# Kernel optimization log

Hardware: AMD Instinct MI355X
Metric: run time of the kernel (lower is better)

## Reference

```python
import jax, jax.numpy as jnp
import numpy as np

B, C, D, H, W = 4, 1, 128, 192, 192


def setup_inputs() -> dict:
    key = jax.random.key(0)
    ks = jax.random.split(key, 8)
    x = jax.random.normal(ks[0], (B, C, D, H, W), jnp.float32)
    y = jax.random.normal(ks[1], (B, C, H, W), jnp.float32)
    rot_0 = jax.random.normal(ks[2], (B, 1), jnp.float32) * 0.1
    rot_1 = jax.random.normal(ks[3], (B, 1), jnp.float32) * 0.1
    rot_2 = jax.random.normal(ks[4], (B, 1), jnp.float32) * 0.1
    trans_1 = jax.random.normal(ks[5], (B, 1), jnp.float32) * 0.05
    trans_2 = jax.random.normal(ks[6], (B, 1), jnp.float32) * 0.05
    center_point = (jnp.tile(jnp.array([[D / 2., H / 2., W / 2.]], jnp.float32), (B, 1))
                    + jax.random.normal(ks[7], (B, 3), jnp.float32))
    return {"x": x, "y": y, "rot_0": rot_0, "rot_1": rot_1, "rot_2": rot_2,
            "trans_1": trans_1, "trans_2": trans_2, "center_point": center_point}


def _euler2mat(a):
    # a: [B,3] angles (z, y, x), ZYX intrinsic composition as in source
    z, y, x = a[:, 0], a[:, 1], a[:, 2]
    cz, sz = jnp.cos(z), jnp.sin(z)
    cy, sy = jnp.cos(y), jnp.sin(y)
    cx, sx = jnp.cos(x), jnp.sin(x)
    o = jnp.ones_like(z)
    zr = jnp.zeros_like(z)
    zmat = jnp.stack([cz, -sz, zr, sz, cz, zr, zr, zr, o], 1).reshape(-1, 3, 3)
    ymat = jnp.stack([cy, zr, sy, zr, o, zr, -sy, zr, cy], 1).reshape(-1, 3, 3)
    xmat = jnp.stack([o, zr, zr, zr, cx, -sx, zr, sx, cx], 1).reshape(-1, 3, 3)
    return zmat @ ymat @ xmat


def _rigid4x4(rot3, t):
    # rot3: [B,3,3], t: [B,3] -> [B,4,4]
    bn = rot3.shape[0]
    top = jnp.concatenate([rot3, t[:, :, None]], axis=-1)          # [B,3,4]
    bot = jnp.broadcast_to(jnp.array([[[0., 0., 0., 1.]]], jnp.float32), (bn, 1, 4))
    return jnp.concatenate([top, bot], axis=1)


def _trans_mat(t):
    bn = t.shape[0]
    eye = jnp.broadcast_to(jnp.eye(3, dtype=jnp.float32), (bn, 3, 3))
    return _rigid4x4(eye, t)


def _affine_grid(mat, shape):
    # mat: [B,4,4]; voxel-coordinate grid (nitorch convention): g = R @ c + t
    d, h, w = shape
    zz, yy, xx = jnp.meshgrid(jnp.arange(d, dtype=jnp.float32),
                              jnp.arange(h, dtype=jnp.float32),
                              jnp.arange(w, dtype=jnp.float32), indexing='ij')
    coords = jnp.stack([zz, yy, xx], axis=-1)                      # [D,H,W,3]
    return (jnp.einsum('dhwj,bij->bdhwi', coords, mat[:, :3, :3])
            + mat[:, None, None, None, :3, 3])                    # [B,D,H,W,3]


def _grid_pull_one(vol, g):
    # vol: [C,D,H,W]; g: [D,H,W,3] voxel coords; trilinear, zero boundary
    d, h, w = vol.shape[1], vol.shape[2], vol.shape[3]
    g0f = jnp.floor(g)
    frac = g - g0f
    g0 = g0f.astype(jnp.int32)
    out = jnp.zeros((vol.shape[0],) + g.shape[:-1], vol.dtype)
    for dz in (0, 1):
        wz = frac[..., 0] if dz else 1. - frac[..., 0]
        iz = g0[..., 0] + dz
        for dy in (0, 1):
            wy = frac[..., 1] if dy else 1. - frac[..., 1]
            iy = g0[..., 1] + dy
            for dx in (0, 1):
                wx = frac[..., 2] if dx else 1. - frac[..., 2]
                ix = g0[..., 2] + dx
                valid = ((iz >= 0) & (iz < d) & (iy >= 0) & (iy < h)
                         & (ix >= 0) & (ix < w)).astype(vol.dtype)
                v = vol[:, jnp.clip(iz, 0, d - 1), jnp.clip(iy, 0, h - 1),
                        jnp.clip(ix, 0, w - 1)]                   # [C,D,H,W]
                out = out + v * (wz * wy * wx * valid)[None]
    return out


def reference(x, y, rot_0, rot_1, rot_2, trans_1, trans_2, center_point):
    d, h, w = x.shape[2], x.shape[3], x.shape[4]
    t1 = _trans_mat(-center_point)
    t2 = _trans_mat(center_point)
    # first translation component is detached*0 -> exact zeros
    trans = jnp.concatenate([jnp.zeros_like(trans_1), trans_1 * h, trans_2 * w], axis=1)
    angles = jnp.concatenate([rot_0, rot_1, rot_2], axis=1)
    rot = _euler2mat(angles)
    rigid = _rigid4x4(rot, trans)
    mat = t2 @ (rigid @ t1)                                        # center-about-point rigid
    grid = _affine_grid(mat, (d, h, w))                            # [B,D,H,W,3]
    x_warp = jax.vmap(_grid_pull_one)(x, grid)                     # [B,C,D,H,W]
    x_2d = jnp.mean(x_warp, axis=2)                                # [B,C,H,W]
    return (x_2d, x_warp, y)
```

## Files before the change

### kernel.cpp

```cpp
#include <hip/hip_runtime.h>

#define Bn 4
#define Dd 128
#define Hh 192
#define Ww 192

#define PLANE (Hh * Ww)
#define VOL   (Dd * PLANE)
#define N2D   (Bn * PLANE)
#define WARP_OFF ((size_t)N2D)
#define Y_OFF (WARP_OFF + (size_t)Bn * VOL)

#define DT 16
#define HT 8
#define WT 32
#define NDB (Dd / DT)
#define NHB (Hh / HT)
#define NWB (Ww / WT)
#define NBLK (Bn * NDB * NHB * NWB)
#define NCH (NDB * 2)

#define SZ 25
#define SY 16
#define SXP 48
#define ZSTRIDE (SY * SXP)
#define LDSF (SZ * ZSTRIDE)

typedef float f2 __attribute__((ext_vector_type(2)));
typedef f2 __attribute__((aligned(4))) f2u;
__device__ __forceinline__ f2 load2(const float* p) { return *(const f2u*)p; }

__device__ __forceinline__ void gload_lds16(const float* g, float* l) {
    __builtin_amdgcn_global_load_lds(
        (const __attribute__((address_space(1))) void*)g,
        (__attribute__((address_space(3))) void*)l,
        16, 0, 0);
}

__global__ __launch_bounds__(256) void tbl_kernel(const float* __restrict__ rot0,
                                                  const float* __restrict__ rot1,
                                                  const float* __restrict__ rot2,
                                                  const float* __restrict__ tr1,
                                                  const float* __restrict__ tr2,
                                                  const float* __restrict__ cp,
                                                  float* __restrict__ tbl) {
    const int id = blockIdx.x * 256 + threadIdx.x;
    if (id >= NBLK) return;
    const int wblk = id % NWB;
    const int t1   = id / NWB;
    const int hblk = t1 % NHB;
    const int t2   = t1 / NHB;
    const int dblk = t2 & (NDB - 1);
    const int b    = t2 >> 3;

    const float z = rot0[b], y = rot1[b], x = rot2[b];
    const float cz = cosf(z), sz = sinf(z);
    const float cy = cosf(y), sy = sinf(y);
    const float cx = cosf(x), sx = sinf(x);
    const float A0 = cz * cy;
    const float B0 = -sz * cx + cz * sy * sx;
    const float C0 = sz * sx + cz * sy * cx;
    const float A1 = sz * cy;
    const float B1 = cz * cx + sz * sy * sx;
    const float C1 = -cz * sx + sz * sy * cx;
    const float A2 = -sy;
    const float B2 = cy * sx;
    const float C2 = cy * cx;
    const float c0 = cp[b * 3 + 0], c1 = cp[b * 3 + 1], c2 = cp[b * 3 + 2];
    const float E0 = -(A0 * c0 + B0 * c1 + C0 * c2) + c0;
    const float E1 = -(A1 * c0 + B1 * c1 + C1 * c2) + tr1[b] * (float)Hh + c1;
    const float E2 = -(A2 * c0 + B2 * c1 + C2 * c2) + tr2[b] * (float)Ww + c2;

    const int d0 = dblk * DT, h0 = hblk * HT, w0 = wblk * WT;
    const float dlo = (float)d0, dhi = (float)(d0 + DT - 1);
    const float hlo = (float)h0, hhi = (float)(h0 + HT - 1);
    const float wlo = (float)w0, whi = (float)(w0 + WT - 1);

    const float loZ = E0 + fminf(A0 * dlo, A0 * dhi) + fminf(B0 * hlo, B0 * hhi) + fminf(C0 * wlo, C0 * whi);
    const float hiZ = E0 + fmaxf(A0 * dlo, A0 * dhi) + fmaxf(B0 * hlo, B0 * hhi) + fmaxf(C0 * wlo, C0 * whi);
    const float loY = E1 + fminf(A1 * dlo, A1 * dhi) + fminf(B1 * hlo, B1 * hhi) + fminf(C1 * wlo, C1 * whi);
    const float hiY = E1 + fmaxf(A1 * dlo, A1 * dhi) + fmaxf(B1 * hlo, B1 * hhi) + fmaxf(C1 * wlo, C1 * whi);
    const float loX = E2 + fminf(A2 * dlo, A2 * dhi) + fminf(B2 * hlo, B2 * hhi) + fminf(C2 * wlo, C2 * whi);
    const float hiX = E2 + fmaxf(A2 * dlo, A2 * dhi) + fmaxf(B2 * hlo, B2 * hhi) + fmaxf(C2 * wlo, C2 * whi);

    const int lz = (int)floorf(loZ) - 1;
    const int hz = (int)floorf(hiZ) + 2;
    const int ly = (int)floorf(loY) - 1;
    const int hy = (int)floorf(hiY) + 2;
    const int lx4 = ((int)floorf(loX) - 1) & ~3;
    const int hx = (int)floorf(hiX) + 2;

    const int hzrel = hz - lz;
    const bool fits = (hzrel <= SZ - 1) && (hy - ly <= SY - 1) && (hx - lx4 <= SXP - 2);
    const bool interior = (loZ >= 0.01f) && (hiZ < (float)(Dd - 1) - 0.01f) &&
                          (loY >= 0.01f) && (hiY < (float)(Hh - 1) - 0.01f) &&
                          (loX >= 0.01f) && (hiX < (float)(Ww - 1) - 0.01f);

    const float bz = E0 + A0 * dlo + B0 * hlo + C0 * wlo - (float)lz;
    const float by = E1 + A1 * dlo + B1 * hlo + C1 * wlo - (float)ly;
    const float bx = E2 + A2 * dlo + B2 * hlo + C2 * wlo - (float)lx4;

    float* T = tbl + (size_t)id * 16;
    T[0] = A0; T[1] = B0; T[2]  = C0; T[3]  = bz;
    T[4] = A1; T[5] = B1; T[6]  = C1; T[7]  = by;
    T[8] = A2; T[9] = B2; T[10] = C2; T[11] = bx;
    int* TI = (int*)T;
    TI[12] = lz; TI[13] = ly; TI[14] = lx4;
    TI[15] = (fits ? 1 : 0) | (interior ? 2 : 0) |
             (b << 2) | (dblk << 4) | (hblk << 7) | (wblk << 12) | (min(hzrel, 127) << 15);
}

template <bool WP>
__global__ __launch_bounds__(512) void warp_tiled(const float* __restrict__ x,
                                                  const float* __restrict__ tbl,
                                                  float* __restrict__ out,
                                                  float* __restrict__ partial) {
    __shared__ __align__(16) float box[LDSF];

    const int g  = blockIdx.x;
    const int wl = (g & 7) * (NBLK / 8) + (g >> 3);

    const float4* T4 = (const float4*)(tbl + (size_t)wl * 16);
    const float4 r0 = T4[0], r1 = T4[1], r2 = T4[2];
    const int4   r3 = ((const int4*)T4)[3];
    const int lz = r3.x, ly = r3.y, lx4 = r3.z, fl = r3.w;
    const bool fits = fl & 1, interior = fl & 2;
    const int b     = (fl >> 2) & 3;
    const int dblk  = (fl >> 4) & 7;
    const int hblk  = (fl >> 7) & 31;
    const int wblk  = (fl >> 12) & 7;
    const int hzrel = (fl >> 15) & 127;
    const int d0 = dblk * DT, h0 = hblk * HT, w0 = wblk * WT;

    const float A0 = r0.x, B0 = r0.y, C0 = r0.z, bz = r0.w;
    const float A1 = r1.x, B1 = r1.y, C1 = r1.z, by = r1.w;
    const float A2 = r2.x, B2 = r2.y, C2 = r2.z, bx = r2.w;

    const int t = threadIdx.x;
    const int w_in = t & 31;
    const int h_in = (t >> 5) & 7;
    const int dq   = t >> 8;
    const int lane = t & 63;
    const int wid  = t >> 6;

    const float fh = (float)h_in, fw = (float)w_in, fdq = (float)(dq * 8);
    const float fz0 = bz + B0 * fh + C0 * fw + A0 * fdq;
    const float fy0 = by + B1 * fh + C1 * fw + A1 * fdq;
    const float fx0 = bx + B2 * fh + C2 * fw + A2 * fdq;

    const float* __restrict__ V = x + (size_t)b * VOL;
    float* __restrict__ obase = out + WARP_OFF + (size_t)b * VOL +
                                (size_t)(d0 + dq * 8) * PLANE +
                                (size_t)(h0 + h_in) * Ww + (w0 + w_in);

    float sum = 0.0f;

    if (fits) {
        const int r0i = lane / 12,             c0i = (lane - r0i * 12) * 4;
        const int i1  = 64 + lane;  const int r1i = i1 / 12, c1i = (i1 - r1i * 12) * 4;
        const int i2  = 128 + lane; const int r2i = i2 / 12, c2i = (i2 - r2i * 12) * 4;
        const int yy0 = ly + r0i, xx0 = lx4 + c0i;
        const int yy1 = ly + r1i, xx1 = lx4 + c1i;
        const int yy2 = ly + r2i, xx2 = lx4 + c2i;
        const bool ok0 = ((unsigned)yy0 < (unsigned)Hh) && ((unsigned)xx0 <= (unsigned)(Ww - 4));
        const bool ok1 = ((unsigned)yy1 < (unsigned)Hh) && ((unsigned)xx1 <= (unsigned)(Ww - 4));
        const bool ok2 = ((unsigned)yy2 < (unsigned)Hh) && ((unsigned)xx2 <= (unsigned)(Ww - 4));
        const int off0 = yy0 * Ww + xx0;
        const int off1 = yy1 * Ww + xx1;
        const int off2 = yy2 * Ww + xx2;

        if (!interior) {
            const float4 z4 = {0.0f, 0.0f, 0.0f, 0.0f};
            for (int i = 4 * t; i < LDSF; i += 4 * 512) *(float4*)&box[i] = z4;
            __syncthreads();
        }

        for (int zrel = wid; zrel <= hzrel; zrel += 8) {
            const int zz = lz + zrel;
            if ((unsigned)zz < (unsigned)Dd) {
                const float* Vz = V + (size_t)zz * PLANE;
                float* Lz = box + zrel * ZSTRIDE;
                if (ok0) gload_lds16(Vz + off0, Lz);
                if (ok1) gload_lds16(Vz + off1, Lz + 256);
                if (ok2) gload_lds16(Vz + off2, Lz + 512);
            }
        }

        int   basev[8];
        float txv[8], tyv[8], tzv[8];
        #pragma unroll
        for (int j = 0; j < 8; ++j) {
            const float fd = (float)j;
            const float gz = fmaf(A0, fd, fz0);
            const float gy = fmaf(A1, fd, fy0);
            const float gx = fmaf(A2, fd, fx0);
            const float fz = floorf(gz), fy = floorf(gy), fx = floorf(gx);
            tzv[j] = gz - fz; tyv[j] = gy - fy; txv[j] = gx - fx;
            basev[j] = (int)fz * ZSTRIDE + (int)fy * SXP + (int)fx;
        }
        __syncthreads();

        #pragma unroll
        for (int j = 0; j < 8; ++j) {
            const int base = basev[j];
            const f2 qa = load2(&box[base]);
            const f2 qb = load2(&box[base + SXP]);
            const f2 qc = load2(&box[base + ZSTRIDE]);
            const f2 qd = load2(&box[base + ZSTRIDE + SXP]);

            const float tx = txv[j], ty = tyv[j], tz = tzv[j];
            const float wx0 = 1.0f - tx, wy0 = 1.0f - ty, wz0 = 1.0f - tz;
            const float v00 = fmaf(wx0, qa.x, tx * qa.y);
            const float v01 = fmaf(wx0, qb.x, tx * qb.y);
            const float v10 = fmaf(wx0, qc.x, tx * qc.y);
            const float v11 = fmaf(wx0, qd.x, tx * qd.y);
            const float vz0 = fmaf(wy0, v00, ty * v01);
            const float vz1 = fmaf(wy0, v10, ty * v11);
            const float val = fmaf(wz0, vz0, tz * vz1);

            __builtin_nontemporal_store(val, obase + (size_t)j * PLANE);
            sum += val;
        }
    } else {
        const float fz0a = fz0 + (float)lz;
        const float fy0a = fy0 + (float)ly;
        const float fx0a = fx0 + (float)lx4;
        #pragma unroll 4
        for (int j = 0; j < 8; ++j) {
            const float fd = (float)j;
            const float gz = fmaf(A0, fd, fz0a);
            const float gy = fmaf(A1, fd, fy0a);
            const float gx = fmaf(A2, fd, fx0a);

            const float fz = floorf(gz), fy = floorf(gy), fx = floorf(gx);
            const float tz = gz - fz, ty = gy - fy, tx = gx - fx;
            const int iz = (int)fz, iy = (int)fy, ix = (int)fx;

            const float wz0 = ((unsigned)iz       < (unsigned)Dd) ? (1.0f - tz) : 0.0f;
            const float wz1 = ((unsigned)(iz + 1) < (unsigned)Dd) ? tz : 0.0f;
            const float wy0 = ((unsigned)iy       < (unsigned)Hh) ? (1.0f - ty) : 0.0f;
            const float wy1 = ((unsigned)(iy + 1) < (unsigned)Hh) ? ty : 0.0f;
            const float wx0 = ((unsigned)ix       < (unsigned)Ww) ? (1.0f - tx) : 0.0f;
            const float wx1 = ((unsigned)(ix + 1) < (unsigned)Ww) ? tx : 0.0f;

            const bool right  = (ix >= Ww - 1);
            const bool leftok = (ix >= 0);
            const float WL = (right ? 0.0f : wx0) + (leftok ? 0.0f : wx1);
            const float WH = (right ? wx0 : 0.0f) + (leftok ? wx1 : 0.0f);

            const int iz0c = min(max(iz, 0), Dd - 1);
            const int iz1c = min(max(iz + 1, 0), Dd - 1);
            const int iy0c = min(max(iy, 0), Hh - 1);
            const int iy1c = min(max(iy + 1, 0), Hh - 1);
            const int ixl  = min(max(ix, 0), Ww - 2);

            const f2 q00 = load2(V + (size_t)iz0c * PLANE + iy0c * Ww + ixl);
            const f2 q01 = load2(V + (size_t)iz0c * PLANE + iy1c * Ww + ixl);
            const f2 q10 = load2(V + (size_t)iz1c * PLANE + iy0c * Ww + ixl);
            const f2 q11 = load2(V + (size_t)iz1c * PLANE + iy1c * Ww + ixl);

            const float v00 = fmaf(WL, q00.x, WH * q00.y);
            const float v01 = fmaf(WL, q01.x, WH * q01.y);
            const float v10 = fmaf(WL, q10.x, WH * q10.y);
            const float v11 = fmaf(WL, q11.x, WH * q11.y);

            const float vz0 = fmaf(wy0, v00, wy1 * v01);
            const float vz1 = fmaf(wy0, v10, wy1 * v11);
            const float val = fmaf(wz0, vz0, wz1 * vz1);

            __builtin_nontemporal_store(val, obase + (size_t)j * PLANE);
            sum += val;
        }
    }

    if (WP) {
        const int ch = dblk * 2 + dq;
        partial[((size_t)(b * NCH + ch) * Hh + (h0 + h_in)) * Ww + (w0 + w_in)] = sum;
    }
}

__global__ __launch_bounds__(256) void reduce_kernel(const float* __restrict__ partial,
                                                     const float* __restrict__ yin,
                                                     float* __restrict__ out) {
    const int idx = blockIdx.x * 256 + threadIdx.x;
    if (idx >= N2D) return;
    const int b = idx / PLANE;
    const int rem = idx - b * PLANE;
    const float* p = partial + (size_t)b * NCH * PLANE + rem;
    float s = 0.0f;
    #pragma unroll
    for (int c = 0; c < NCH; ++c) s += p[(size_t)c * PLANE];
    out[idx] = s * (1.0f / (float)Dd);
    out[Y_OFF + idx] = yin[idx];
}

__global__ __launch_bounds__(256) void reduce_fallback_kernel(const float* __restrict__ yin,
                                                              float* __restrict__ out) {
    const int idx = blockIdx.x * 256 + threadIdx.x;
    if (idx >= N2D) return;
    const int b = idx / PLANE;
    const int rem = idx - b * PLANE;
    const float* p = out + WARP_OFF + (size_t)b * VOL + rem;
    float s = 0.0f;
    #pragma unroll 8
    for (int d = 0; d < Dd; ++d) s += p[(size_t)d * PLANE];
    out[idx] = s * (1.0f / (float)Dd);
    out[Y_OFF + idx] = yin[idx];
}

extern "C" void kernel_launch(void* const* d_in, const int* in_sizes, int n_in,
                              void* d_out, int out_size, void* d_ws, size_t ws_size,
                              hipStream_t stream) {
    const float* x    = (const float*)d_in[0];
    const float* yin  = (const float*)d_in[1];
    const float* rot0 = (const float*)d_in[2];
    const float* rot1 = (const float*)d_in[3];
    const float* rot2 = (const float*)d_in[4];
    const float* tr1  = (const float*)d_in[5];
    const float* tr2  = (const float*)d_in[6];
    const float* cp   = (const float*)d_in[7];

    float* tbl = (float*)d_ws;
    float* partial = tbl + (size_t)NBLK * 16;
    const size_t need = ((size_t)NBLK * 16 + (size_t)Bn * NCH * PLANE) * sizeof(float);

    tbl_kernel<<<(NBLK + 255) / 256, 256, 0, stream>>>(rot0, rot1, rot2, tr1, tr2, cp, tbl);

    if (ws_size >= need) {
        warp_tiled<true><<<NBLK, 512, 0, stream>>>(x, tbl, (float*)d_out, partial);
        reduce_kernel<<<(N2D + 255) / 256, 256, 0, stream>>>(partial, yin, (float*)d_out);
    } else {
        warp_tiled<false><<<NBLK, 512, 0, stream>>>(x, tbl, (float*)d_out, partial);
        reduce_fallback_kernel<<<(N2D + 255) / 256, 256, 0, stream>>>(yin, (float*)d_out);
    }
}
```

Measured before the change: 50.64 us.

## Split each warp tile into two depth phases with smaller LDS box

The per-block 16-deep tile is now processed in two sequential 8-deep phases, each with its own bounding-box table entry. This shrinks the LDS staging box from 25 to 17 z-slices, which raises how many blocks fit per CU and tightens the loaded halo per phase. The cost is an extra barrier between phases and serialized load/compute inside each block. The reduce kernel is also vectorized to float4 loads and stores.

```diff
diff --git a/kernel.cpp b/kernel.cpp
--- a/kernel.cpp
+++ b/kernel.cpp
@@ -18,9 +18,10 @@
 #define NHB (Hh / HT)
 #define NWB (Ww / WT)
 #define NBLK (Bn * NDB * NHB * NWB)
+#define NTBL (NBLK * 2)
 #define NCH (NDB * 2)
 
-#define SZ 25
+#define SZ 17
 #define SY 16
 #define SXP 48
 #define ZSTRIDE (SY * SXP)
@@ -45,9 +46,11 @@
                                                   const float* __restrict__ cp,
                                                   float* __restrict__ tbl) {
     const int id = blockIdx.x * 256 + threadIdx.x;
-    if (id >= NBLK) return;
-    const int wblk = id % NWB;
-    const int t1   = id / NWB;
+    if (id >= NTBL) return;
+    const int wl    = id >> 1;
+    const int phase = id & 1;
+    const int wblk = wl % NWB;
+    const int t1   = wl / NWB;
     const int hblk = t1 % NHB;
     const int t2   = t1 / NHB;
     const int dblk = t2 & (NDB - 1);
@@ -71,8 +74,9 @@
     const float E1 = -(A1 * c0 + B1 * c1 + C1 * c2) + tr1[b] * (float)Hh + c1;
     const float E2 = -(A2 * c0 + B2 * c1 + C2 * c2) + tr2[b] * (float)Ww + c2;
 
-    const int d0 = dblk * DT, h0 = hblk * HT, w0 = wblk * WT;
-    const float dlo = (float)d0, dhi = (float)(d0 + DT - 1);
+    const int d0 = dblk * DT + phase * 8;
+    const int h0 = hblk * HT, w0 = wblk * WT;
+    const float dlo = (float)d0, dhi = (float)(d0 + 7);
     const float hlo = (float)h0, hhi = (float)(h0 + HT - 1);
     const float wlo = (float)w0, whi = (float)(w0 + WT - 1);
 
@@ -120,22 +124,6 @@
     const int g  = blockIdx.x;
     const int wl = (g & 7) * (NBLK / 8) + (g >> 3);
 
-    const float4* T4 = (const float4*)(tbl + (size_t)wl * 16);
-    const float4 r0 = T4[0], r1 = T4[1], r2 = T4[2];
-    const int4   r3 = ((const int4*)T4)[3];
-    const int lz = r3.x, ly = r3.y, lx4 = r3.z, fl = r3.w;
-    const bool fits = fl & 1, interior = fl & 2;
-    const int b     = (fl >> 2) & 3;
-    const int dblk  = (fl >> 4) & 7;
-    const int hblk  = (fl >> 7) & 31;
-    const int wblk  = (fl >> 12) & 7;
-    const int hzrel = (fl >> 15) & 127;
-    const int d0 = dblk * DT, h0 = hblk * HT, w0 = wblk * WT;
-
-    const float A0 = r0.x, B0 = r0.y, C0 = r0.z, bz = r0.w;
-    const float A1 = r1.x, B1 = r1.y, C1 = r1.z, by = r1.w;
-    const float A2 = r2.x, B2 = r2.y, C2 = r2.z, bx = r2.w;
-
     const int t = threadIdx.x;
     const int w_in = t & 31;
     const int h_in = (t >> 5) & 7;
@@ -143,155 +131,186 @@
     const int lane = t & 63;
     const int wid  = t >> 6;
 
-    const float fh = (float)h_in, fw = (float)w_in, fdq = (float)(dq * 8);
-    const float fz0 = bz + B0 * fh + C0 * fw + A0 * fdq;
-    const float fy0 = by + B1 * fh + C1 * fw + A1 * fdq;
-    const float fx0 = bx + B2 * fh + C2 * fw + A2 * fdq;
-
-    const float* __restrict__ V = x + (size_t)b * VOL;
-    float* __restrict__ obase = out + WARP_OFF + (size_t)b * VOL +
-                                (size_t)(d0 + dq * 8) * PLANE +
-                                (size_t)(h0 + h_in) * Ww + (w0 + w_in);
+    const int r0i = lane / 12,             c0i = (lane - r0i * 12) * 4;
+    const int i1  = 64 + lane;  const int r1i = i1 / 12, c1i = (i1 - r1i * 12) * 4;
+    const int i2  = 128 + lane; const int r2i = i2 / 12, c2i = (i2 - r2i * 12) * 4;
 
     float sum = 0.0f;
-
-    if (fits) {
-        const int r0i = lane / 12,             c0i = (lane - r0i * 12) * 4;
-        const int i1  = 64 + lane;  const int r1i = i1 / 12, c1i = (i1 - r1i * 12) * 4;
-        const int i2  = 128 + lane; const int r2i = i2 / 12, c2i = (i2 - r2i * 12) * 4;
-        const int yy0 = ly + r0i, xx0 = lx4 + c0i;
-        const int yy1 = ly + r1i, xx1 = lx4 + c1i;
-        const int yy2 = ly + r2i, xx2 = lx4 + c2i;
-        const bool ok0 = ((unsigned)yy0 < (unsigned)Hh) && ((unsigned)xx0 <= (unsigned)(Ww - 4));
-        const bool ok1 = ((unsigned)yy1 < (unsigned)Hh) && ((unsigned)xx1 <= (unsigned)(Ww - 4));
-        const bool ok2 = ((unsigned)yy2 < (unsigned)Hh) && ((unsigned)xx2 <= (unsigned)(Ww - 4));
-        const int off0 = yy0 * Ww + xx0;
-        const int off1 = yy1 * Ww + xx1;
-        const int off2 = yy2 * Ww + xx2;
-
-        if (!interior) {
-            const float4 z4 = {0.0f, 0.0f, 0.0f, 0.0f};
-            for (int i = 4 * t; i < LDSF; i += 4 * 512) *(float4*)&box[i] = z4;
+    int bO = 0, dblkO = 0, h0O = 0, w0O = 0;
+
+    #pragma unroll 1
+    for (int ph = 0; ph < 2; ++ph) {
+        const float4* T4 = (const float4*)(tbl + ((size_t)wl * 2 + ph) * 16);
+        const float4 r0 = T4[0], r1 = T4[1], r2 = T4[2];
+        const int4   r3 = ((const int4*)T4)[3];
+        const int lz = r3.x, ly = r3.y, lx4 = r3.z, fl = r3.w;
+        const bool fits = fl & 1, interior = fl & 2;
+        const int b     = (fl >> 2) & 3;
+        const int dblk  = (fl >> 4) & 7;
+        const int hblk  = (fl >> 7) & 31;
+        const int wblk  = (fl >> 12) & 7;
+        const int hzrel = (fl >> 15) & 127;
+        const int h0 = hblk * HT, w0 = wblk * WT;
+        const int d0 = dblk * DT + ph * 8;
+        bO = b; dblkO = dblk; h0O = h0; w0O = w0;
+
+        const float A0 = r0.x, B0 = r0.y, C0 = r0.z, bz = r0.w;
+        const float A1 = r1.x, B1 = r1.y, C1 = r1.z, by = r1.w;
+        const float A2 = r2.x, B2 = r2.y, C2 = r2.z, bx = r2.w;
+
+        const float fh = (float)h_in, fw = (float)w_in, fdq = (float)(dq * 4);
+        const float fz0 = bz + B0 * fh + C0 * fw + A0 * fdq;
+        const float fy0 = by + B1 * fh + C1 * fw + A1 * fdq;
+        const float fx0 = bx + B2 * fh + C2 * fw + A2 * fdq;
+
+        const float* __restrict__ V = x + (size_t)b * VOL;
+        float* __restrict__ obase = out + WARP_OFF + (size_t)b * VOL +
+                                    (size_t)(d0 + dq * 4) * PLANE +
+                                    (size_t)(h0 + h_in) * Ww + (w0 + w_in);
+
+        if (fits) {
+            const int yy0 = ly + r0i, xx0 = lx4 + c0i;
+            const int yy1 = ly + r1i, xx1 = lx4 + c1i;
+            const int yy2 = ly + r2i, xx2 = lx4 + c2i;
+            const bool ok0 = ((unsigned)yy0 < (unsigned)Hh) && ((unsigned)xx0 <= (unsigned)(Ww - 4));
+            const bool ok1 = ((unsigned)yy1 < (unsigned)Hh) && ((unsigned)xx1 <= (unsigned)(Ww - 4));
+            const bool ok2 = ((unsigned)yy2 < (unsigned)Hh) && ((unsigned)xx2 <= (unsigned)(Ww - 4));
+            const int off0 = yy0 * Ww + xx0;
+            const int off1 = yy1 * Ww + xx1;
+            const int off2 = yy2 * Ww + xx2;
+
+            if (!interior) {
+                const float4 z4 = {0.0f, 0.0f, 0.0f, 0.0f};
+                for (int i = 4 * t; i < LDSF; i += 4 * 512) *(float4*)&box[i] = z4;
+                __syncthreads();
+            }
+
+            for (int zrel = wid; zrel <= hzrel; zrel += 8) {
+                const int zz = lz + zrel;
+                if ((unsigned)zz < (unsigned)Dd) {
+                    const float* Vz = V + (size_t)zz * PLANE;
+                    float* Lz = box + zrel * ZSTRIDE;
+                    if (ok0) gload_lds16(Vz + off0, Lz);
+                    if (ok1) gload_lds16(Vz + off1, Lz + 256);
+                    if (ok2) gload_lds16(Vz + off2, Lz + 512);
+                }
+            }
+
+            int   basev[4];
+            float txv[4], tyv[4], tzv[4];
+            #pragma unroll
+            for (int j = 0; j < 4; ++j) {
+                const float fd = (float)j;
+                const float gz = fmaf(A0, fd, fz0);
+                const float gy = fmaf(A1, fd, fy0);
+                const float gx = fmaf(A2, fd, fx0);
+                const float fz = floorf(gz), fy = floorf(gy), fx = floorf(gx);
+                tzv[j] = gz - fz; tyv[j] = gy - fy; txv[j] = gx - fx;
+                basev[j] = (int)fz * ZSTRIDE + (int)fy * SXP + (int)fx;
+            }
             __syncthreads();
+
+            #pragma unroll
+            for (int j = 0; j < 4; ++j) {
+                const int base = basev[j];
+                const f2 qa = load2(&box[base]);
+                const f2 qb = load2(&box[base + SXP]);
+                const f2 qc = load2(&box[base + ZSTRIDE]);
+                const f2 qd = load2(&box[base + ZSTRIDE + SXP]);
+
+                const float tx = txv[j], ty = tyv[j], tz = tzv[j];
+                const float wx0 = 1.0f - tx, wy0 = 1.0f - ty, wz0 = 1.0f - tz;
+                const float v00 = fmaf(wx0, qa.x, tx * qa.y);
+                const float v01 = fmaf(wx0, qb.x, tx * qb.y);
+                const float v10 = fmaf(wx0, qc.x, tx * qc.y);
+                const float v11 = fmaf(wx0, qd.x, tx * qd.y);
+                const float vz0 = fmaf(wy0, v00, ty * v01);
+                const float vz1 = fmaf(wy0, v10, ty * v11);
+                const float val = fmaf(wz0, vz0, tz * vz1);
+
+                __builtin_nontemporal_store(val, obase + (size_t)j * PLANE);
+                sum += val;
+            }
+        } else {
+            const float fz0a = fz0 + (float)lz;
+            const float fy0a = fy0 + (float)ly;
+            const float fx0a = fx0 + (float)lx4;
+            #pragma unroll
+            for (int j = 0; j < 4; ++j) {
+                const float fd = (float)j;
+                const float gz = fmaf(A0, fd, fz0a);
+                const float gy = fmaf(A1, fd, fy0a);
+                const float gx = fmaf(A2, fd, fx0a);
+
+                const float fz = floorf(gz), fy = floorf(gy), fx = floorf(gx);
+                const float tz = gz - fz, ty = gy - fy, tx = gx - fx;
+                const int iz = (int)fz, iy = (int)fy, ix = (int)fx;
+
+                const float wz0 = ((unsigned)iz       < (unsigned)Dd) ? (1.0f - tz) : 0.0f;
+                const float wz1 = ((unsigned)(iz + 1) < (unsigned)Dd) ? tz : 0.0f;
+                const float wy0 = ((unsigned)iy       < (unsigned)Hh) ? (1.0f - ty) : 0.0f;
+                const float wy1 = ((unsigned)(iy + 1) < (unsigned)Hh) ? ty : 0.0f;
+                const float wx0 = ((unsigned)ix       < (unsigned)Ww) ? (1.0f - tx) : 0.0f;
+                const float wx1 = ((unsigned)(ix + 1) < (unsigned)Ww) ? tx : 0.0f;
+
+                const bool right  = (ix >= Ww - 1);
+                const bool leftok = (ix >= 0);
+                const float WL = (right ? 0.0f : wx0) + (leftok ? 0.0f : wx1);
+                const float WH = (right ? wx0 : 0.0f) + (leftok ? wx1 : 0.0f);
+
+                const int iz0c = min(max(iz, 0), Dd - 1);
+                const int iz1c = min(max(iz + 1, 0), Dd - 1);
+                const int iy0c = min(max(iy, 0), Hh - 1);
+                const int iy1c = min(max(iy + 1, 0), Hh - 1);
+                const int ixl  = min(max(ix, 0), Ww - 2);
+
+                const f2 q00 = load2(V + (size_t)iz0c * PLANE + iy0c * Ww + ixl);
+                const f2 q01 = load2(V + (size_t)iz0c * PLANE + iy1c * Ww + ixl);
+                const f2 q10 = load2(V + (size_t)iz1c * PLANE + iy0c * Ww + ixl);
+                const f2 q11 = load2(V + (size_t)iz1c * PLANE + iy1c * Ww + ixl);
+
+                const float v00 = fmaf(WL, q00.x, WH * q00.y);
+                const float v01 = fmaf(WL, q01.x, WH * q01.y);
+                const float v10 = fmaf(WL, q10.x, WH * q10.y);
+                const float v11 = fmaf(WL, q11.x, WH * q11.y);
+
+                const float vz0 = fmaf(wy0, v00, wy1 * v01);
+                const float vz1 = fmaf(wy0, v10, wy1 * v11);
+                const float val = fmaf(wz0, vz0, wz1 * vz1);
+
+                __builtin_nontemporal_store(val, obase + (size_t)j * PLANE);
+                sum += val;
+            }
         }
 
-        for (int zrel = wid; zrel <= hzrel; zrel += 8) {
-            const int zz = lz + zrel;
-            if ((unsigned)zz < (unsigned)Dd) {
-                const float* Vz = V + (size_t)zz * PLANE;
-                float* Lz = box + zrel * ZSTRIDE;
-                if (ok0) gload_lds16(Vz + off0, Lz);
-                if (ok1) gload_lds16(Vz + off1, Lz + 256);
-                if (ok2) gload_lds16(Vz + off2, Lz + 512);
-            }
-        }
-
-        int   basev[8];
-        float txv[8], tyv[8], tzv[8];
-        #pragma unroll
-        for (int j = 0; j < 8; ++j) {
-            const float fd = (float)j;
-            const float gz = fmaf(A0, fd, fz0);
-            const float gy = fmaf(A1, fd, fy0);
-            const float gx = fmaf(A2, fd, fx0);
-            const float fz = floorf(gz), fy = floorf(gy), fx = floorf(gx);
-            tzv[j] = gz - fz; tyv[j] = gy - fy; txv[j] = gx - fx;
-            basev[j] = (int)fz * ZSTRIDE + (int)fy * SXP + (int)fx;
-        }
-        __syncthreads();
-
-        #pragma unroll
-        for (int j = 0; j < 8; ++j) {
-            const int base = basev[j];
-            const f2 qa = load2(&box[base]);
-            const f2 qb = load2(&box[base + SXP]);
-            const f2 qc = load2(&box[base + ZSTRIDE]);
-            const f2 qd = load2(&box[base + ZSTRIDE + SXP]);
-
-            const float tx = txv[j], ty = tyv[j], tz = tzv[j];
-            const float wx0 = 1.0f - tx, wy0 = 1.0f - ty, wz0 = 1.0f - tz;
-            const float v00 = fmaf(wx0, qa.x, tx * qa.y);
-            const float v01 = fmaf(wx0, qb.x, tx * qb.y);
-            const float v10 = fmaf(wx0, qc.x, tx * qc.y);
-            const float v11 = fmaf(wx0, qd.x, tx * qd.y);
-            const float vz0 = fmaf(wy0, v00, ty * v01);
-            const float vz1 = fmaf(wy0, v10, ty * v11);
-            const float val = fmaf(wz0, vz0, tz * vz1);
-
-            __builtin_nontemporal_store(val, obase + (size_t)j * PLANE);
-            sum += val;
-        }
-    } else {
-        const float fz0a = fz0 + (float)lz;
-        const float fy0a = fy0 + (float)ly;
-        const float fx0a = fx0 + (float)lx4;
-        #pragma unroll 4
-        for (int j = 0; j < 8; ++j) {
-            const float fd = (float)j;
-            const float gz = fmaf(A0, fd, fz0a);
-            const float gy = fmaf(A1, fd, fy0a);
-            const float gx = fmaf(A2, fd, fx0a);
-
-            const float fz = floorf(gz), fy = floorf(gy), fx = floorf(gx);
-            const float tz = gz - fz, ty = gy - fy, tx = gx - fx;
-            const int iz = (int)fz, iy = (int)fy, ix = (int)fx;
-
-            const float wz0 = ((unsigned)iz       < (unsigned)Dd) ? (1.0f - tz) : 0.0f;
-            const float wz1 = ((unsigned)(iz + 1) < (unsigned)Dd) ? tz : 0.0f;
-            const float wy0 = ((unsigned)iy       < (unsigned)Hh) ? (1.0f - ty) : 0.0f;
-            const float wy1 = ((unsigned)(iy + 1) < (unsigned)Hh) ? ty : 0.0f;
-            const float wx0 = ((unsigned)ix       < (unsigned)Ww) ? (1.0f - tx) : 0.0f;
-            const float wx1 = ((unsigned)(ix + 1) < (unsigned)Ww) ? tx : 0.0f;
-
-            const bool right  = (ix >= Ww - 1);
-            const bool leftok = (ix >= 0);
-            const float WL = (right ? 0.0f : wx0) + (leftok ? 0.0f : wx1);
-            const float WH = (right ? wx0 : 0.0f) + (leftok ? wx1 : 0.0f);
-
-            const int iz0c = min(max(iz, 0), Dd - 1);
-            const int iz1c = min(max(iz + 1, 0), Dd - 1);
-            const int iy0c = min(max(iy, 0), Hh - 1);
-            const int iy1c = min(max(iy + 1, 0), Hh - 1);
-            const int ixl  = min(max(ix, 0), Ww - 2);
-
-            const f2 q00 = load2(V + (size_t)iz0c * PLANE + iy0c * Ww + ixl);
-            const f2 q01 = load2(V + (size_t)iz0c * PLANE + iy1c * Ww + ixl);
-            const f2 q10 = load2(V + (size_t)iz1c * PLANE + iy0c * Ww + ixl);
-            const f2 q11 = load2(V + (size_t)iz1c * PLANE + iy1c * Ww + ixl);
-
-            const float v00 = fmaf(WL, q00.x, WH * q00.y);
-            const float v01 = fmaf(WL, q01.x, WH * q01.y);
-            const float v10 = fmaf(WL, q10.x, WH * q10.y);
-            const float v11 = fmaf(WL, q11.x, WH * q11.y);
-
-            const float vz0 = fmaf(wy0, v00, wy1 * v01);
-            const float vz1 = fmaf(wy0, v10, wy1 * v11);
-            const float val = fmaf(wz0, vz0, wz1 * vz1);
-
-            __builtin_nontemporal_store(val, obase + (size_t)j * PLANE);
-            sum += val;
-        }
+        if (ph == 0) __syncthreads();
     }
 
     if (WP) {
-        const int ch = dblk * 2 + dq;
-        partial[((size_t)(b * NCH + ch) * Hh + (h0 + h_in)) * Ww + (w0 + w_in)] = sum;
+        const int ch = dblkO * 2 + dq;
+        partial[((size_t)(bO * NCH + ch) * Hh + (h0O + h_in)) * Ww + (w0O + w_in)] = sum;
     }
 }
 
 __global__ __launch_bounds__(256) void reduce_kernel(const float* __restrict__ partial,
                                                      const float* __restrict__ yin,
                                                      float* __restrict__ out) {
-    const int idx = blockIdx.x * 256 + threadIdx.x;
-    if (idx >= N2D) return;
+    const int q = blockIdx.x * 256 + threadIdx.x;
+    if (q >= N2D / 4) return;
+    const int idx = q * 4;
     const int b = idx / PLANE;
     const int rem = idx - b * PLANE;
     const float* p = partial + (size_t)b * NCH * PLANE + rem;
-    float s = 0.0f;
+    float4 s = {0.0f, 0.0f, 0.0f, 0.0f};
     #pragma unroll
-    for (int c = 0; c < NCH; ++c) s += p[(size_t)c * PLANE];
-    out[idx] = s * (1.0f / (float)Dd);
-    out[Y_OFF + idx] = yin[idx];
+    for (int c = 0; c < NCH; ++c) {
+        const float4 v = *(const float4*)(p + (size_t)c * PLANE);
+        s.x += v.x; s.y += v.y; s.z += v.z; s.w += v.w;
+    }
+    const float inv = 1.0f / (float)Dd;
+    s.x *= inv; s.y *= inv; s.z *= inv; s.w *= inv;
+    *(float4*)(out + idx) = s;
+    *(float4*)(out + Y_OFF + idx) = *(const float4*)(yin + idx);
 }
 
 __global__ __launch_bounds__(256) void reduce_fallback_kernel(const float* __restrict__ yin,
@@ -321,14 +340,14 @@
     const float* cp   = (const float*)d_in[7];
 
     float* tbl = (float*)d_ws;
-    float* partial = tbl + (size_t)NBLK * 16;
-    const size_t need = ((size_t)NBLK * 16 + (size_t)Bn * NCH * PLANE) * sizeof(float);
-
-    tbl_kernel<<<(NBLK + 255) / 256, 256, 0, stream>>>(rot0, rot1, rot2, tr1, tr2, cp, tbl);
+    float* partial = tbl + (size_t)NTBL * 16;
+    const size_t need = ((size_t)NTBL * 16 + (size_t)Bn * NCH * PLANE) * sizeof(float);
+
+    tbl_kernel<<<(NTBL + 255) / 256, 256, 0, stream>>>(rot0, rot1, rot2, tr1, tr2, cp, tbl);
 
     if (ws_size >= need) {
         warp_tiled<true><<<NBLK, 512, 0, stream>>>(x, tbl, (float*)d_out, partial);
-        reduce_kernel<<<(N2D + 255) / 256, 256, 0, stream>>>(partial, yin, (float*)d_out);
+        reduce_kernel<<<(N2D / 4 + 255) / 256, 256, 0, stream>>>(partial, yin, (float*)d_out);
     } else {
         warp_tiled<false><<<NBLK, 512, 0, stream>>>(x, tbl, (float*)d_out, partial);
         reduce_fallback_kernel<<<(N2D + 255) / 256, 256, 0, stream>>>(yin, (float*)d_out);
```

After: 60.05 us. 18.6% more time.
